# Kernel optimization log

Hardware: AMD Instinct MI355X
Metric: run time of the kernel (lower is better)

## Reference

```python
import jax, jax.numpy as jnp
import numpy as np

INPUT_DIM = 256
OUTPUT_DIM = 256
DEGREE = 7


def setup_inputs() -> dict:
    key = jax.random.key(0)
    k1, k2 = jax.random.split(key)
    x = jax.random.normal(k1, (16, 2048, INPUT_DIM), dtype=jnp.float32)
    std = 1.0 / (INPUT_DIM * (DEGREE + 1))
    hermite_coeffs = std * jax.random.normal(k2, (INPUT_DIM, OUTPUT_DIM, DEGREE + 1), dtype=jnp.float32)
    return {"x": x, "hermite_coeffs": hermite_coeffs}


def reference(x, hermite_coeffs):
    a, b, c = x.shape
    degree = hermite_coeffs.shape[2] - 1
    xf = jnp.tanh(x.reshape(-1, c))  # [N, input_dim]
    hs = [jnp.ones_like(xf)]
    if degree > 0:
        hs.append(2.0 * xf)
    for i in range(2, degree + 1):
        hs.append(2.0 * xf * hs[-1] - 2.0 * (i - 1) * hs[-2])
    hermite = jnp.stack(hs, axis=-1)  # [N, input_dim, degree+1]
    y = jnp.einsum('bid,iod->bo', hermite, hermite_coeffs)
    return y.reshape(a, b, hermite_coeffs.shape[1])
```

## Files before the change

### kernel.cpp

```cpp
#include <hip/hip_runtime.h>
#include <hip/hip_bf16.h>
#include <math.h>

#define INPUT_DIM 256
#define OUT_DIM   256
#define NDEG      8
#define KTOT      (INPUT_DIM * NDEG)
#define NROWS     (16 * 2048)

#define BM  128
#define BK  64
#define NK  (KTOT / BK)
#define CHUNK_ELEMS 16384

typedef __bf16 bf16x8 __attribute__((ext_vector_type(8)));
typedef float  f32x16 __attribute__((ext_vector_type(16)));

__global__ __launch_bounds__(256) void reorder_coeffs(const float* __restrict__ C,
                                                      __bf16* __restrict__ Bt) {
    int g = blockIdx.x * 256 + threadIdx.x;
    int i = g >> 8;
    int o = g & 255;
    const float4* src = (const float4*)(C + (size_t)i * (OUT_DIM * NDEG) + o * NDEG);
    float4 a = src[0];
    float4 b = src[1];
    bf16x8 v;
    v[0] = (__bf16)a.x; v[1] = (__bf16)a.y; v[2] = (__bf16)a.z; v[3] = (__bf16)a.w;
    v[4] = (__bf16)b.x; v[5] = (__bf16)b.y; v[6] = (__bf16)b.z; v[7] = (__bf16)b.w;
    int kc = i >> 3;
    int p  = i & 7;
    int s  = p >> 1;
    int hh = p & 1;
    int cc = o >> 6;
    int ni = (o >> 5) & 1;
    int l31 = o & 31;
    size_t dst = (size_t)kc * CHUNK_ELEMS + (s * 4 + cc) * 1024 + ni * 512 + hh * 256 + l31 * 8;
    *(bf16x8*)(Bt + dst) = v;
}

__device__ __forceinline__ bf16x8 featurize(float xs) {
    float e = __expf(2.0f * xs);
    float t = 1.0f - 2.0f / (e + 1.0f);
    bf16x8 v;
    float hm2 = 1.0f;
    float hm1 = 2.0f * t;
    v[0] = (__bf16)hm2;
    v[1] = (__bf16)hm1;
    #pragma unroll
    for (int d = 2; d < 8; ++d) {
        float h = 2.0f * t * hm1 - 2.0f * (float)(d - 1) * hm2;
        v[d] = (__bf16)h;
        hm2 = hm1; hm1 = h;
    }
    return v;
}

#define BARRIER() do {                                             \
    asm volatile("s_waitcnt lgkmcnt(0)" ::: "memory");             \
    __builtin_amdgcn_s_barrier();                                  \
    asm volatile("" ::: "memory");                                 \
} while (0)

__global__ __launch_bounds__(512, 2) void hermite_mfma(const float* __restrict__ x,
                                                       const __bf16* __restrict__ Bt,
                                                       float* __restrict__ out) {
    __shared__ __align__(16) __bf16 Alds[2][8192];

    const int tid  = threadIdx.x;
    const int bm   = blockIdx.x;
    const int wave = tid >> 6;
    const int mr   = wave >> 2;
    const int c    = wave & 3;
    const int lane = tid & 63;
    const int l31  = lane & 31;
    const int h    = lane >> 5;

    const int m  = tid & 127;
    const int pg = tid >> 7;
    const float* xptr = x + (size_t)(bm * BM + m) * INPUT_DIM + pg * 2;

    const __bf16* bbase = Bt + (size_t)c * 1024 + lane * 8;

    f32x16 acc[2][2] = {};
    bf16x8 bfr0[4][2];
    bf16x8 bfr1[4][2];

    float2 xv = *(const float2*)(xptr);
    #pragma unroll
    for (int s = 0; s < 4; ++s)
        #pragma unroll
        for (int ni = 0; ni < 2; ++ni)
            bfr0[s][ni] = *(const bf16x8*)(bbase + s * 4096 + ni * 512);
    *(bf16x8*)(&Alds[0][(pg * 2 + 0) * 1024 + m * 8]) = featurize(xv.x);
    *(bf16x8*)(&Alds[0][(pg * 2 + 1) * 1024 + m * 8]) = featurize(xv.y);
    xv = *(const float2*)(xptr + 8);
    BARRIER();

#define STEP(KC, CUR, NXT, CB, NB)                                           \
    {                                                                        \
        if ((KC) + 1 < NK) {                                                 \
            const __bf16* g = bbase + (size_t)((KC) + 1) * CHUNK_ELEMS;      \
            _Pragma("unroll")                                                \
            for (int s = 0; s < 4; ++s) {                                    \
                NXT[s][0] = *(const bf16x8*)(g + s * 4096);                  \
                NXT[s][1] = *(const bf16x8*)(g + s * 4096 + 512);            \
            }                                                                \
            *(bf16x8*)(&Alds[NB][(pg * 2 + 0) * 1024 + m * 8]) = featurize(xv.x); \
            *(bf16x8*)(&Alds[NB][(pg * 2 + 1) * 1024 + m * 8]) = featurize(xv.y); \
            int kn = ((KC) + 2 < NK) ? (KC) + 2 : NK - 1;                    \
            xv = *(const float2*)(xptr + kn * 8);                            \
        }                                                                    \
        _Pragma("unroll")                                                    \
        for (int s = 0; s < 4; ++s) {                                        \
            bf16x8 af0 = *(const bf16x8*)(&Alds[CB][(2 * s + h) * 1024 + mr * 512 + l31 * 8]);       \
            bf16x8 af1 = *(const bf16x8*)(&Alds[CB][(2 * s + h) * 1024 + mr * 512 + 256 + l31 * 8]); \
            acc[0][0] = __builtin_amdgcn_mfma_f32_32x32x16_bf16(af0, CUR[s][0], acc[0][0], 0, 0, 0); \
            acc[0][1] = __builtin_amdgcn_mfma_f32_32x32x16_bf16(af0, CUR[s][1], acc[0][1], 0, 0, 0); \
            acc[1][0] = __builtin_amdgcn_mfma_f32_32x32x16_bf16(af1, CUR[s][0], acc[1][0], 0, 0, 0); \
            acc[1][1] = __builtin_amdgcn_mfma_f32_32x32x16_bf16(af1, CUR[s][1], acc[1][1], 0, 0, 0); \
        }                                                                    \
        BARRIER();                                                           \
    }

    for (int kc2 = 0; kc2 < NK; kc2 += 2) {
        STEP(kc2,     bfr0, bfr1, 0, 1);
        STEP(kc2 + 1, bfr1, bfr0, 1, 0);
    }
#undef STEP

    #pragma unroll
    for (int mi = 0; mi < 2; ++mi)
        #pragma unroll
        for (int ni = 0; ni < 2; ++ni) {
            #pragma unroll
            for (int r = 0; r < 16; ++r) {
                int rl  = (r & 3) + 8 * (r >> 2) + 4 * h;
                int row = bm * BM + mr * 64 + mi * 32 + rl;
                out[(size_t)row * OUT_DIM + c * 64 + ni * 32 + l31] = acc[mi][ni][r];
            }
        }
}

extern "C" void kernel_launch(void* const* d_in, const int* in_sizes, int n_in,
                              void* d_out, int out_size, void* d_ws, size_t ws_size,
                              hipStream_t stream) {
    const float* x = (const float*)d_in[0];
    const float* C = (const float*)d_in[1];
    float* out = (float*)d_out;
    __bf16* Bt = (__bf16*)d_ws;

    reorder_coeffs<<<dim3((INPUT_DIM * OUT_DIM) / 256), dim3(256), 0, stream>>>(C, Bt);
    hermite_mfma<<<dim3(NROWS / BM), dim3(512), 0, stream>>>(x, Bt, out);
}
```

Baseline: 120.4 us.

## Batch four K-chunks per barrier with larger double-buffered LDS featurization

```diff
diff --git a/kernel.cpp b/kernel.cpp
--- a/kernel.cpp
+++ b/kernel.cpp
@@ -11,6 +11,8 @@
 #define BM  128
 #define BK  64
 #define NK  (KTOT / BK)
+#define SUPER 4
+#define NSUP  (NK / SUPER)
 #define CHUNK_ELEMS 16384
 
 typedef __bf16 bf16x8 __attribute__((ext_vector_type(8)));
@@ -64,7 +66,7 @@
 __global__ __launch_bounds__(512, 2) void hermite_mfma(const float* __restrict__ x,
                                                        const __bf16* __restrict__ Bt,
                                                        float* __restrict__ out) {
-    __shared__ __align__(16) __bf16 Alds[2][8192];
+    __shared__ __align__(16) __bf16 Alds[2][SUPER * 8192];
 
     const int tid  = threadIdx.x;
     const int bm   = blockIdx.x;
@@ -77,7 +79,7 @@
 
     const int m  = tid & 127;
     const int pg = tid >> 7;
-    const float* xptr = x + (size_t)(bm * BM + m) * INPUT_DIM + pg * 2;
+    const float* xptr = x + (size_t)(bm * BM + m) * INPUT_DIM + pg * 8;
 
     const __bf16* bbase = Bt + (size_t)c * 1024 + lane * 8;
 
@@ -85,48 +87,70 @@
     bf16x8 bfr0[4][2];
     bf16x8 bfr1[4][2];
 
-    float2 xv = *(const float2*)(xptr);
-    #pragma unroll
-    for (int s = 0; s < 4; ++s)
-        #pragma unroll
-        for (int ni = 0; ni < 2; ++ni)
-            bfr0[s][ni] = *(const bf16x8*)(bbase + s * 4096 + ni * 512);
-    *(bf16x8*)(&Alds[0][(pg * 2 + 0) * 1024 + m * 8]) = featurize(xv.x);
-    *(bf16x8*)(&Alds[0][(pg * 2 + 1) * 1024 + m * 8]) = featurize(xv.y);
-    xv = *(const float2*)(xptr + 8);
+#define BLOAD(DST, KC)                                                       \
+    if ((KC) < NK) {                                                         \
+        const __bf16* g = bbase + (size_t)(KC) * CHUNK_ELEMS;                \
+        _Pragma("unroll")                                                    \
+        for (int s = 0; s < 4; ++s) {                                        \
+            DST[s][0] = *(const bf16x8*)(g + s * 4096);                      \
+            DST[s][1] = *(const bf16x8*)(g + s * 4096 + 512);                \
+        }                                                                    \
+    }
+
+#define FEATW(NB, J, XS)                                                     \
+    *(bf16x8*)(&Alds[NB][pg * 8192 + (J) * 1024 + m * 8]) = featurize(XS)
+
+#define CHUNK_COMPUTE(CB, CC, CUR)                                           \
+    _Pragma("unroll")                                                        \
+    for (int s4 = 0; s4 < 4; ++s4) {                                         \
+        bf16x8 af0 = *(const bf16x8*)(&Alds[CB][(CC) * 8192 + (2 * s4 + h) * 1024 + mr * 512 + l31 * 8]);       \
+        bf16x8 af1 = *(const bf16x8*)(&Alds[CB][(CC) * 8192 + (2 * s4 + h) * 1024 + mr * 512 + 256 + l31 * 8]); \
+        acc[0][0] = __builtin_amdgcn_mfma_f32_32x32x16_bf16(af0, CUR[s4][0], acc[0][0], 0, 0, 0); \
+        acc[0][1] = __builtin_amdgcn_mfma_f32_32x32x16_bf16(af0, CUR[s4][1], acc[0][1], 0, 0, 0); \
+        acc[1][0] = __builtin_amdgcn_mfma_f32_32x32x16_bf16(af1, CUR[s4][0], acc[1][0], 0, 0, 0); \
+        acc[1][1] = __builtin_amdgcn_mfma_f32_32x32x16_bf16(af1, CUR[s4][1], acc[1][1], 0, 0, 0); \
+    }
+
+    float4 xq0 = *(const float4*)(xptr);
+    float4 xq1 = *(const float4*)(xptr + 4);
+    BLOAD(bfr0, 0);
+    float4 xa0 = *(const float4*)(xptr + 32);
+    float4 xa1 = *(const float4*)(xptr + 36);
+    float4 xb0 = xa0, xb1 = xa1;
+    FEATW(0, 0, xq0.x); FEATW(0, 1, xq0.y); FEATW(0, 2, xq0.z); FEATW(0, 3, xq0.w);
+    FEATW(0, 4, xq1.x); FEATW(0, 5, xq1.y); FEATW(0, 6, xq1.z); FEATW(0, 7, xq1.w);
     BARRIER();
 
-#define STEP(KC, CUR, NXT, CB, NB)                                           \
+#define SUPER_STEP(S, CB, NB, XC0, XC1, XN0, XN1)                            \
     {                                                                        \
-        if ((KC) + 1 < NK) {                                                 \
-            const __bf16* g = bbase + (size_t)((KC) + 1) * CHUNK_ELEMS;      \
-            _Pragma("unroll")                                                \
-            for (int s = 0; s < 4; ++s) {                                    \
-                NXT[s][0] = *(const bf16x8*)(g + s * 4096);                  \
-                NXT[s][1] = *(const bf16x8*)(g + s * 4096 + 512);            \
-            }                                                                \
-            *(bf16x8*)(&Alds[NB][(pg * 2 + 0) * 1024 + m * 8]) = featurize(xv.x); \
-            *(bf16x8*)(&Alds[NB][(pg * 2 + 1) * 1024 + m * 8]) = featurize(xv.y); \
-            int kn = ((KC) + 2 < NK) ? (KC) + 2 : NK - 1;                    \
-            xv = *(const float2*)(xptr + kn * 8);                            \
+        const bool dofeat = (S) + 1 < NSUP;                                  \
+        BLOAD(bfr1, (S) * 4 + 1);                                            \
+        if (dofeat) { FEATW(NB, 0, XC0.x); FEATW(NB, 1, XC0.y); }            \
+        CHUNK_COMPUTE(CB, 0, bfr0);                                          \
+        BLOAD(bfr0, (S) * 4 + 2);                                            \
+        if (dofeat) { FEATW(NB, 2, XC0.z); FEATW(NB, 3, XC0.w); }            \
+        CHUNK_COMPUTE(CB, 1, bfr1);                                          \
+        BLOAD(bfr1, (S) * 4 + 3);                                            \
+        if (dofeat) { FEATW(NB, 4, XC1.x); FEATW(NB, 5, XC1.y); }            \
+        CHUNK_COMPUTE(CB, 2, bfr0);                                          \
+        BLOAD(bfr0, (S) * 4 + 4);                                            \
+        if (dofeat) { FEATW(NB, 6, XC1.z); FEATW(NB, 7, XC1.w); }            \
+        if ((S) + 2 < NSUP) {                                                \
+            XN0 = *(const float4*)(xptr + ((S) + 2) * 32);                   \
+            XN1 = *(const float4*)(xptr + ((S) + 2) * 32 + 4);               \
         }                                                                    \
-        _Pragma("unroll")                                                    \
-        for (int s = 0; s < 4; ++s) {                                        \
-            bf16x8 af0 = *(const bf16x8*)(&Alds[CB][(2 * s + h) * 1024 + mr * 512 + l31 * 8]);       \
-            bf16x8 af1 = *(const bf16x8*)(&Alds[CB][(2 * s + h) * 1024 + mr * 512 + 256 + l31 * 8]); \
-            acc[0][0] = __builtin_amdgcn_mfma_f32_32x32x16_bf16(af0, CUR[s][0], acc[0][0], 0, 0, 0); \
-            acc[0][1] = __builtin_amdgcn_mfma_f32_32x32x16_bf16(af0, CUR[s][1], acc[0][1], 0, 0, 0); \
-            acc[1][0] = __builtin_amdgcn_mfma_f32_32x32x16_bf16(af1, CUR[s][0], acc[1][0], 0, 0, 0); \
-            acc[1][1] = __builtin_amdgcn_mfma_f32_32x32x16_bf16(af1, CUR[s][1], acc[1][1], 0, 0, 0); \
-        }                                                                    \
+        CHUNK_COMPUTE(CB, 3, bfr1);                                          \
         BARRIER();                                                           \
     }
 
-    for (int kc2 = 0; kc2 < NK; kc2 += 2) {
-        STEP(kc2,     bfr0, bfr1, 0, 1);
-        STEP(kc2 + 1, bfr1, bfr0, 1, 0);
+    for (int sp = 0; sp < NSUP; sp += 2) {
+        SUPER_STEP(sp,     0, 1, xa0, xa1, xb0, xb1);
+        SUPER_STEP(sp + 1, 1, 0, xb0, xb1, xa0, xa1);
     }
-#undef STEP
+#undef SUPER_STEP
+#undef CHUNK_COMPUTE
+#undef FEATW
+#undef BLOAD
 
     #pragma unroll
     for (int mi = 0; mi < 2; ++mi)
```

Measured after the change: 115.1 us. 4.5% less time.

## Featurize A fragments in registers per wave, drop LDS staging and barriers

Applied to the files above, without the earlier changes.

```diff
diff --git a/kernel.cpp b/kernel.cpp
--- a/kernel.cpp
+++ b/kernel.cpp
@@ -15,6 +15,7 @@
 
 typedef __bf16 bf16x8 __attribute__((ext_vector_type(8)));
 typedef float  f32x16 __attribute__((ext_vector_type(16)));
+typedef float  f32x4  __attribute__((ext_vector_type(4)));
 
 __global__ __launch_bounds__(256) void reorder_coeffs(const float* __restrict__ C,
                                                       __bf16* __restrict__ Bt) {
@@ -29,8 +30,8 @@
     v[4] = (__bf16)b.x; v[5] = (__bf16)b.y; v[6] = (__bf16)b.z; v[7] = (__bf16)b.w;
     int kc = i >> 3;
     int p  = i & 7;
-    int s  = p >> 1;
-    int hh = p & 1;
+    int hh = p >> 2;
+    int s  = p & 3;
     int cc = o >> 6;
     int ni = (o >> 5) & 1;
     int l31 = o & 31;
@@ -55,17 +56,9 @@
     return v;
 }
 
-#define BARRIER() do {                                             \
-    asm volatile("s_waitcnt lgkmcnt(0)" ::: "memory");             \
-    __builtin_amdgcn_s_barrier();                                  \
-    asm volatile("" ::: "memory");                                 \
-} while (0)
-
 __global__ __launch_bounds__(512, 2) void hermite_mfma(const float* __restrict__ x,
                                                        const __bf16* __restrict__ Bt,
                                                        float* __restrict__ out) {
-    __shared__ __align__(16) __bf16 Alds[2][8192];
-
     const int tid  = threadIdx.x;
     const int bm   = blockIdx.x;
     const int wave = tid >> 6;
@@ -75,9 +68,9 @@
     const int l31  = lane & 31;
     const int h    = lane >> 5;
 
-    const int m  = tid & 127;
-    const int pg = tid >> 7;
-    const float* xptr = x + (size_t)(bm * BM + m) * INPUT_DIM + pg * 2;
+    const int row0 = bm * BM + mr * 64 + l31;
+    const float* xr0 = x + (size_t)row0 * INPUT_DIM + h * 4;
+    const float* xr1 = xr0 + (size_t)32 * INPUT_DIM;
 
     const __bf16* bbase = Bt + (size_t)c * 1024 + lane * 8;
 
@@ -85,48 +78,45 @@
     bf16x8 bfr0[4][2];
     bf16x8 bfr1[4][2];
 
-    float2 xv = *(const float2*)(xptr);
-    #pragma unroll
-    for (int s = 0; s < 4; ++s)
-        #pragma unroll
-        for (int ni = 0; ni < 2; ++ni)
-            bfr0[s][ni] = *(const bf16x8*)(bbase + s * 4096 + ni * 512);
-    *(bf16x8*)(&Alds[0][(pg * 2 + 0) * 1024 + m * 8]) = featurize(xv.x);
-    *(bf16x8*)(&Alds[0][(pg * 2 + 1) * 1024 + m * 8]) = featurize(xv.y);
-    xv = *(const float2*)(xptr + 8);
-    BARRIER();
+#define BLOAD(DST, KC)                                                       \
+    {                                                                        \
+        const __bf16* g = bbase + (size_t)(KC) * CHUNK_ELEMS;                \
+        _Pragma("unroll")                                                    \
+        for (int s = 0; s < 4; ++s) {                                        \
+            DST[s][0] = *(const bf16x8*)(g + s * 4096);                      \
+            DST[s][1] = *(const bf16x8*)(g + s * 4096 + 512);                \
+        }                                                                    \
+    }
 
-#define STEP(KC, CUR, NXT, CB, NB)                                           \
+    f32x4 xa0 = *(const f32x4*)(xr0);
+    f32x4 xa1 = *(const f32x4*)(xr1);
+    BLOAD(bfr0, 0);
+    f32x4 xb0 = xa0, xb1 = xa1;
+
+#define STEP(KC, CUR, NXT, XC0, XC1, XN0, XN1)                               \
     {                                                                        \
         if ((KC) + 1 < NK) {                                                 \
-            const __bf16* g = bbase + (size_t)((KC) + 1) * CHUNK_ELEMS;      \
-            _Pragma("unroll")                                                \
-            for (int s = 0; s < 4; ++s) {                                    \
-                NXT[s][0] = *(const bf16x8*)(g + s * 4096);                  \
-                NXT[s][1] = *(const bf16x8*)(g + s * 4096 + 512);            \
-            }                                                                \
-            *(bf16x8*)(&Alds[NB][(pg * 2 + 0) * 1024 + m * 8]) = featurize(xv.x); \
-            *(bf16x8*)(&Alds[NB][(pg * 2 + 1) * 1024 + m * 8]) = featurize(xv.y); \
-            int kn = ((KC) + 2 < NK) ? (KC) + 2 : NK - 1;                    \
-            xv = *(const float2*)(xptr + kn * 8);                            \
+            BLOAD(NXT, (KC) + 1);                                            \
+            XN0 = *(const f32x4*)(xr0 + ((KC) + 1) * 8);                     \
+            XN1 = *(const f32x4*)(xr1 + ((KC) + 1) * 8);                     \
         }                                                                    \
         _Pragma("unroll")                                                    \
         for (int s = 0; s < 4; ++s) {                                        \
-            bf16x8 af0 = *(const bf16x8*)(&Alds[CB][(2 * s + h) * 1024 + mr * 512 + l31 * 8]);       \
-            bf16x8 af1 = *(const bf16x8*)(&Alds[CB][(2 * s + h) * 1024 + mr * 512 + 256 + l31 * 8]); \
+            bf16x8 af0 = featurize(XC0[s]);                                  \
+            bf16x8 af1 = featurize(XC1[s]);                                  \
             acc[0][0] = __builtin_amdgcn_mfma_f32_32x32x16_bf16(af0, CUR[s][0], acc[0][0], 0, 0, 0); \
             acc[0][1] = __builtin_amdgcn_mfma_f32_32x32x16_bf16(af0, CUR[s][1], acc[0][1], 0, 0, 0); \
             acc[1][0] = __builtin_amdgcn_mfma_f32_32x32x16_bf16(af1, CUR[s][0], acc[1][0], 0, 0, 0); \
             acc[1][1] = __builtin_amdgcn_mfma_f32_32x32x16_bf16(af1, CUR[s][1], acc[1][1], 0, 0, 0); \
         }                                                                    \
-        BARRIER();                                                           \
     }
 
     for (int kc2 = 0; kc2 < NK; kc2 += 2) {
-        STEP(kc2,     bfr0, bfr1, 0, 1);
-        STEP(kc2 + 1, bfr1, bfr0, 1, 0);
+        STEP(kc2,     bfr0, bfr1, xa0, xa1, xb0, xb1);
+        STEP(kc2 + 1, bfr1, bfr0, xb0, xb1, xa0, xa1);
     }
 #undef STEP
+#undef BLOAD
 
     #pragma unroll
     for (int mi = 0; mi < 2; ++mi)
```

Result: slower. 136.8 us (+13.6%).

## Warp-specialize featurization into producer waves with four-chunk LDS superstages

Applied to the files above, without the earlier changes.

```diff
diff --git a/kernel.cpp b/kernel.cpp
--- a/kernel.cpp
+++ b/kernel.cpp
@@ -11,6 +11,8 @@
 #define BM  128
 #define BK  64
 #define NK  (KTOT / BK)
+#define SUPER 4
+#define NSUP  (NK / SUPER)
 #define CHUNK_ELEMS 16384
 
 typedef __bf16 bf16x8 __attribute__((ext_vector_type(8)));
@@ -61,84 +63,127 @@
     asm volatile("" ::: "memory");                                 \
 } while (0)
 
-__global__ __launch_bounds__(512, 2) void hermite_mfma(const float* __restrict__ x,
+__global__ __launch_bounds__(768, 3) void hermite_mfma(const float* __restrict__ x,
                                                        const __bf16* __restrict__ Bt,
                                                        float* __restrict__ out) {
-    __shared__ __align__(16) __bf16 Alds[2][8192];
+    __shared__ __align__(16) __bf16 Alds[2][SUPER * 8192];
 
     const int tid  = threadIdx.x;
     const int bm   = blockIdx.x;
     const int wave = tid >> 6;
-    const int mr   = wave >> 2;
-    const int c    = wave & 3;
-    const int lane = tid & 63;
-    const int l31  = lane & 31;
-    const int h    = lane >> 5;
 
-    const int m  = tid & 127;
-    const int pg = tid >> 7;
-    const float* xptr = x + (size_t)(bm * BM + m) * INPUT_DIM + pg * 2;
+    if (wave < 8) {
+        const int mr   = wave >> 2;
+        const int c    = wave & 3;
+        const int lane = tid & 63;
+        const int l31  = lane & 31;
+        const int h    = lane >> 5;
 
-    const __bf16* bbase = Bt + (size_t)c * 1024 + lane * 8;
+        const __bf16* bbase = Bt + (size_t)c * 1024 + lane * 8;
 
-    f32x16 acc[2][2] = {};
-    bf16x8 bfr0[4][2];
-    bf16x8 bfr1[4][2];
+        f32x16 acc[2][2] = {};
+        bf16x8 bfr0[4][2];
+        bf16x8 bfr1[4][2];
 
-    float2 xv = *(const float2*)(xptr);
-    #pragma unroll
-    for (int s = 0; s < 4; ++s)
-        #pragma unroll
-        for (int ni = 0; ni < 2; ++ni)
-            bfr0[s][ni] = *(const bf16x8*)(bbase + s * 4096 + ni * 512);
-    *(bf16x8*)(&Alds[0][(pg * 2 + 0) * 1024 + m * 8]) = featurize(xv.x);
-    *(bf16x8*)(&Alds[0][(pg * 2 + 1) * 1024 + m * 8]) = featurize(xv.y);
-    xv = *(const float2*)(xptr + 8);
-    BARRIER();
-
-#define STEP(KC, CUR, NXT, CB, NB)                                           \
-    {                                                                        \
-        if ((KC) + 1 < NK) {                                                 \
-            const __bf16* g = bbase + (size_t)((KC) + 1) * CHUNK_ELEMS;      \
+#define BLOAD(DST, KC)                                                       \
+        if ((KC) < NK) {                                                     \
+            const __bf16* g = bbase + (size_t)(KC) * CHUNK_ELEMS;            \
             _Pragma("unroll")                                                \
             for (int s = 0; s < 4; ++s) {                                    \
-                NXT[s][0] = *(const bf16x8*)(g + s * 4096);                  \
-                NXT[s][1] = *(const bf16x8*)(g + s * 4096 + 512);            \
+                DST[s][0] = *(const bf16x8*)(g + s * 4096);                  \
+                DST[s][1] = *(const bf16x8*)(g + s * 4096 + 512);            \
             }                                                                \
-            *(bf16x8*)(&Alds[NB][(pg * 2 + 0) * 1024 + m * 8]) = featurize(xv.x); \
-            *(bf16x8*)(&Alds[NB][(pg * 2 + 1) * 1024 + m * 8]) = featurize(xv.y); \
-            int kn = ((KC) + 2 < NK) ? (KC) + 2 : NK - 1;                    \
-            xv = *(const float2*)(xptr + kn * 8);                            \
-        }                                                                    \
-        _Pragma("unroll")                                                    \
-        for (int s = 0; s < 4; ++s) {                                        \
-            bf16x8 af0 = *(const bf16x8*)(&Alds[CB][(2 * s + h) * 1024 + mr * 512 + l31 * 8]);       \
-            bf16x8 af1 = *(const bf16x8*)(&Alds[CB][(2 * s + h) * 1024 + mr * 512 + 256 + l31 * 8]); \
-            acc[0][0] = __builtin_amdgcn_mfma_f32_32x32x16_bf16(af0, CUR[s][0], acc[0][0], 0, 0, 0); \
-            acc[0][1] = __builtin_amdgcn_mfma_f32_32x32x16_bf16(af0, CUR[s][1], acc[0][1], 0, 0, 0); \
-            acc[1][0] = __builtin_amdgcn_mfma_f32_32x32x16_bf16(af1, CUR[s][0], acc[1][0], 0, 0, 0); \
-            acc[1][1] = __builtin_amdgcn_mfma_f32_32x32x16_bf16(af1, CUR[s][1], acc[1][1], 0, 0, 0); \
-        }                                                                    \
-        BARRIER();                                                           \
+        }
+
+#define MFMA4(AF0, AF1, CURS)                                                \
+        acc[0][0] = __builtin_amdgcn_mfma_f32_32x32x16_bf16(AF0, CURS[0], acc[0][0], 0, 0, 0); \
+        acc[0][1] = __builtin_amdgcn_mfma_f32_32x32x16_bf16(AF0, CURS[1], acc[0][1], 0, 0, 0); \
+        acc[1][0] = __builtin_amdgcn_mfma_f32_32x32x16_bf16(AF1, CURS[0], acc[1][0], 0, 0, 0); \
+        acc[1][1] = __builtin_amdgcn_mfma_f32_32x32x16_bf16(AF1, CURS[1], acc[1][1], 0, 0, 0);
+
+#define CSTEP(KC, CC, CUR, NXT)                                              \
+        {                                                                    \
+            const __bf16* ab = &Alds[CB][(CC) * 8192 + mr * 512 + l31 * 8];  \
+            bf16x8 a0 = *(const bf16x8*)(ab + (0 + h) * 1024);               \
+            bf16x8 a1 = *(const bf16x8*)(ab + (0 + h) * 1024 + 256);         \
+            bf16x8 a2 = *(const bf16x8*)(ab + (2 + h) * 1024);               \
+            bf16x8 a3 = *(const bf16x8*)(ab + (2 + h) * 1024 + 256);         \
+            bf16x8 a4 = *(const bf16x8*)(ab + (4 + h) * 1024);               \
+            bf16x8 a5 = *(const bf16x8*)(ab + (4 + h) * 1024 + 256);         \
+            bf16x8 a6 = *(const bf16x8*)(ab + (6 + h) * 1024);               \
+            bf16x8 a7 = *(const bf16x8*)(ab + (6 + h) * 1024 + 256);         \
+            BLOAD(NXT, (KC) + 1);                                            \
+            __builtin_amdgcn_s_setprio(1);                                   \
+            MFMA4(a0, a1, CUR[0]); MFMA4(a2, a3, CUR[1]);                    \
+            MFMA4(a4, a5, CUR[2]); MFMA4(a6, a7, CUR[3]);                    \
+            __builtin_amdgcn_s_setprio(0);                                   \
+        }
+
+        BLOAD(bfr0, 0);
+        BARRIER();
+
+        #pragma unroll 2
+        for (int S = 0; S < NSUP; ++S) {
+            const int CB = S & 1;
+            const int k0 = S * 4;
+            CSTEP(k0 + 0, 0, bfr0, bfr1);
+            CSTEP(k0 + 1, 1, bfr1, bfr0);
+            CSTEP(k0 + 2, 2, bfr0, bfr1);
+            CSTEP(k0 + 3, 3, bfr1, bfr0);
+            BARRIER();
+        }
+#undef CSTEP
+#undef MFMA4
+#undef BLOAD
+
+        #pragma unroll
+        for (int mi = 0; mi < 2; ++mi)
+            #pragma unroll
+            for (int ni = 0; ni < 2; ++ni) {
+                #pragma unroll
+                for (int r = 0; r < 16; ++r) {
+                    int rl  = (r & 3) + 8 * (r >> 2) + 4 * h;
+                    int row = bm * BM + mr * 64 + mi * 32 + rl;
+                    out[(size_t)row * OUT_DIM + c * 64 + ni * 32 + l31] = acc[mi][ni][r];
+                }
+            }
+    } else {
+        const int ptid = tid - 512;
+        const int m    = ptid & 127;
+        const int g    = ptid >> 7;
+        const float* xptr = x + (size_t)(bm * BM + m) * INPUT_DIM + g * 16;
+
+#define PFEAT4(NB, J0, Q)                                                    \
+        *(bf16x8*)(&Alds[NB][(g * 16 + (J0) + 0) * 1024 + m * 8]) = featurize(Q.x); \
+        *(bf16x8*)(&Alds[NB][(g * 16 + (J0) + 1) * 1024 + m * 8]) = featurize(Q.y); \
+        *(bf16x8*)(&Alds[NB][(g * 16 + (J0) + 2) * 1024 + m * 8]) = featurize(Q.z); \
+        *(bf16x8*)(&Alds[NB][(g * 16 + (J0) + 3) * 1024 + m * 8]) = featurize(Q.w);
+
+        {
+            float4 q0 = *(const float4*)(xptr);
+            float4 q1 = *(const float4*)(xptr + 4);
+            float4 q2 = *(const float4*)(xptr + 8);
+            float4 q3 = *(const float4*)(xptr + 12);
+            PFEAT4(0, 0,  q0); PFEAT4(0, 4,  q1);
+            PFEAT4(0, 8,  q2); PFEAT4(0, 12, q3);
+        }
+        BARRIER();
+
+        for (int S = 0; S < NSUP; ++S) {
+            if (S + 1 < NSUP) {
+                const int NB = (S + 1) & 1;
+                const float* xs = xptr + (S + 1) * 32;
+                float4 q0 = *(const float4*)(xs);
+                float4 q1 = *(const float4*)(xs + 4);
+                float4 q2 = *(const float4*)(xs + 8);
+                float4 q3 = *(const float4*)(xs + 12);
+                PFEAT4(NB, 0,  q0); PFEAT4(NB, 4,  q1);
+                PFEAT4(NB, 8,  q2); PFEAT4(NB, 12, q3);
+            }
+            BARRIER();
+        }
+#undef PFEAT4
     }
-
-    for (int kc2 = 0; kc2 < NK; kc2 += 2) {
-        STEP(kc2,     bfr0, bfr1, 0, 1);
-        STEP(kc2 + 1, bfr1, bfr0, 1, 0);
-    }
-#undef STEP
-
-    #pragma unroll
-    for (int mi = 0; mi < 2; ++mi)
-        #pragma unroll
-        for (int ni = 0; ni < 2; ++ni) {
-            #pragma unroll
-            for (int r = 0; r < 16; ++r) {
-                int rl  = (r & 3) + 8 * (r >> 2) + 4 * h;
-                int row = bm * BM + mr * 64 + mi * 32 + rl;
-                out[(size_t)row * OUT_DIM + c * 64 + ni * 32 + l31] = acc[mi][ni][r];
-            }
-        }
 }
 
 extern "C" void kernel_launch(void* const* d_in, const int* in_sizes, int n_in,
@@ -150,5 +195,5 @@
     __bf16* Bt = (__bf16*)d_ws;
 
     reorder_coeffs<<<dim3((INPUT_DIM * OUT_DIM) / 256), dim3(256), 0, stream>>>(C, Bt);
-    hermite_mfma<<<dim3(NROWS / BM), dim3(512), 0, stream>>>(x, Bt, out);
+    hermite_mfma<<<dim3(NROWS / BM), dim3(768), 0, stream>>>(x, Bt, out);
 }
```

Result: slower. 181.6 us (+50.8%).
